# Kernel tuning notes

Hardware: AMD Instinct MI355X
Metric: run time of the kernel (lower is better)

Reference implementation:

```python
import jax, jax.numpy as jnp
import numpy as np

N = 100000      # nodes
E = 1600000     # edges
F_IN = 128      # feature_dim
H = 128         # hidden_dim
OUT = 40        # out_dim


def setup_inputs() -> dict:
    key = jax.random.key(0)
    ks = jax.random.split(key, 8)
    x = jax.random.normal(ks[0], (N, F_IN), dtype=jnp.float32)
    edge_index = jax.random.randint(ks[1], (2, E), 0, N)
    def lin(k, fan_in, fan_out):
        kw, kb = jax.random.split(k)
        s = 1.0 / np.sqrt(fan_in)
        W = jax.random.uniform(kw, (fan_in, fan_out), jnp.float32, -s, s)
        b = jax.random.uniform(kb, (fan_out,), jnp.float32, -s, s)
        return W, b
    W1, b1 = lin(ks[2], F_IN, H)
    W2, b2 = lin(ks[3], H, H)
    Wc, bc = lin(ks[4], H, OUT)
    return {"x": x, "W1": W1, "b1": b1, "W2": W2, "b2": b2,
            "Wc": Wc, "bc": bc, "edge_index": edge_index}


def gcn_conv(x, W, b, src, dst, n):
    # GCNConv: D^{-1/2} (A + I) D^{-1/2} X W + b  (self loops already in src/dst)
    h = x @ W                                            # [n, out]
    deg = jax.ops.segment_sum(jnp.ones(src.shape[0], h.dtype), dst,
                              num_segments=n)            # [n]
    dinv = jnp.where(deg > 0, jax.lax.rsqrt(deg), 0.0)
    norm = dinv[src] * dinv[dst]                         # [E+n]
    msg = h[src] * norm[:, None]                         # gather + scale
    out = jax.ops.segment_sum(msg, dst, num_segments=n)  # scatter-add
    return out + b


def reference(x, W1, b1, W2, b2, Wc, bc, edge_index):
    loops = jnp.arange(N, dtype=edge_index.dtype)
    src = jnp.concatenate([edge_index[0], loops])
    dst = jnp.concatenate([edge_index[1], loops])
    # mode=0, eval mode: dropout is identity
    out1 = jax.nn.relu(gcn_conv(x, W1, b1, src, dst, N))
    out2 = jax.nn.relu(gcn_conv(out1, W2, b2, src, dst, N))
    return (out2 + out1) @ Wc + bc
```

## Files before the change

### kernel.cpp

```cpp
#include <hip/hip_runtime.h>
#include <stdint.h>


#define HID 128
#define OUTD 40
#define BSH 8
#define BCAP 6144
#define CAPSH 13
#define EPB 8192
#define NBMAX 512

typedef __attribute__((ext_vector_type(8))) short short8;
typedef __attribute__((ext_vector_type(4))) float f32x4;
typedef __attribute__((ext_vector_type(2))) float f32x2;

__device__ inline uint16_t f32_to_bf16(float f) {
    uint32_t u = __float_as_uint(f);
    uint32_t r = u + 0x7FFFu + ((u >> 16) & 1u);
    return (uint16_t)(r >> 16);
}
__device__ inline uint32_t pack_bf16x2(float lo, float hi) {
    return (uint32_t)f32_to_bf16(lo) | ((uint32_t)f32_to_bf16(hi) << 16);
}
__device__ inline float bf_lo(uint32_t u) { return __uint_as_float(u << 16); }
__device__ inline float bf_hi(uint32_t u) { return __uint_as_float(u & 0xFFFF0000u); }
__device__ inline f32x2 up2(uint32_t u) {
    f32x2 r;
    r.x = __uint_as_float(u << 16);
    r.y = __uint_as_float(u & 0xFFFF0000u);
    return r;
}


__global__ __launch_bounds__(256) void gnn_bucket_scatter_k(const int* __restrict__ edges,
                                                            int* __restrict__ pcur,
                                                            uint32_t* __restrict__ pairbuf,
                                                            int E, int NB) {
    __shared__ int hist[NBMAX];
    int e0 = blockIdx.x * EPB;
    int e1 = min(E, e0 + EPB);
    for (int b = threadIdx.x; b < NB; b += 256) hist[b] = 0;
    __syncthreads();
    for (int e = e0 + threadIdx.x; e < e1; e += 256)
        atomicAdd(&hist[edges[E + e] >> BSH], 1);
    __syncthreads();
    for (int b = threadIdx.x; b < NB; b += 256) {
        int c = hist[b];
        hist[b] = (c > 0) ? (atomicAdd(&pcur[b], c) + (b << CAPSH)) : 0;
    }
    __syncthreads();
    for (int e = e0 + threadIdx.x; e < e1; e += 256) {
        int src = edges[e];
        int dst = edges[E + e];
        int pos = atomicAdd(&hist[dst >> BSH], 1);
        pairbuf[pos] = ((uint32_t)(dst & 255) << 24) | (uint32_t)src;
    }
}

__global__ __launch_bounds__(512) void gnn_scan_wsw_k(const int* __restrict__ pcur,
                                                      int* __restrict__ bucketoff,
                                                      const float* __restrict__ W1,
                                                      const float* __restrict__ W2,
                                                      uint16_t* __restrict__ w1s,
                                                      uint16_t* __restrict__ w2s,
                                                      int n, int NB) {
    if (blockIdx.x == 0) {
        __shared__ int s[512];
        int t = threadIdx.x;
        int v = 0;
        if (t < NB) v = pcur[t] + min(256, n - (t << BSH));
        s[t] = v;
        __syncthreads();
        for (int off = 1; off < 512; off <<= 1) {
            int x = 0;
            if (t >= off) x = s[t - off];
            __syncthreads();
            if (t >= off) s[t] += x;
            __syncthreads();
        }
        if (t <= NB) bucketoff[t] = s[t] - v;
    } else if (threadIdx.x < 256) {
        int wb = blockIdx.x - 1;
        const float* W = (wb < 8) ? W1 : W2;
        uint16_t* O = (wb < 8) ? w1s : w2s;
        int t = (wb & 7) * 256 + threadIdx.x;
        int lane = t & 63;
        int ksct = t >> 6;
        int nn = (ksct >> 2) * 16 + (lane & 15);
        int k0 = (ksct & 3) * 32 + (lane >> 4) * 8;
        uint32_t d[4];
#pragma unroll
        for (int j = 0; j < 4; ++j)
            d[j] = pack_bf16x2(W[(size_t)(k0 + 2 * j) * HID + nn],
                               W[(size_t)(k0 + 2 * j + 1) * HID + nn]);
        *(uint4*)(O + (size_t)t * 8) = make_uint4(d[0], d[1], d[2], d[3]);
    }
}

__global__ __launch_bounds__(256) void gnn_build_csr_k(const uint32_t* __restrict__ pairbuf,
                                                       const int* __restrict__ bucketoff,
                                                       int* __restrict__ rowptr,
                                                       float* __restrict__ dinv,
                                                       int* __restrict__ colidx, int n) {
    __shared__ int deg[256];
    __shared__ int scn[256];
    __shared__ int colbuf[BCAP];
    int b = blockIdx.x;
    int nb0 = b << BSH;
    int nb1 = min(n, nb0 + 256);
    int nn = nb1 - nb0;
    int segbeg = bucketoff[b];
    int segend = bucketoff[b + 1];
    int seglen = segend - segbeg;
    int pairbeg = b << CAPSH;
    int npairs = seglen - nn;
    int t = threadIdx.x;

    deg[t] = 0;
    __syncthreads();
    for (int p = t; p < npairs; p += 256)
        atomicAdd(&deg[pairbuf[pairbeg + p] >> 24], 1);
    __syncthreads();

    int d = (t < nn) ? deg[t] : 0;
    int v = (t < nn) ? d + 1 : 0;
    scn[t] = v;
    __syncthreads();
    for (int off = 1; off < 256; off <<= 1) {
        int x = 0;
        if (t >= off) x = scn[t - off];
        __syncthreads();
        if (t >= off) scn[t] += x;
        __syncthreads();
    }
    int rel = scn[t] - v;
    if (t < nn) {
        rowptr[nb0 + t + 1] = segbeg + scn[t];
        dinv[nb0 + t] = rsqrtf((float)(d + 1));
    }
    if (t == 0) rowptr[nb0] = segbeg;
    __syncthreads();

    if (seglen <= BCAP) {
        if (t < nn) {
            colbuf[rel] = nb0 + t;
            deg[t] = rel + 1;
        }
        __syncthreads();
        for (int p = t; p < npairs; p += 256) {
            uint32_t pr = pairbuf[pairbeg + p];
            int pos = atomicAdd(&deg[pr >> 24], 1);
            colbuf[pos] = (int)(pr & 0xFFFFFFu);
        }
        __syncthreads();
        for (int i = t; i < seglen; i += 256)
            colidx[segbeg + i] = colbuf[i];
    } else {
        if (t < nn) {
            colidx[segbeg + rel] = nb0 + t;
            deg[t] = rel + 1;
        }
        __syncthreads();
        for (int p = t; p < npairs; p += 256) {
            uint32_t pr = pairbuf[pairbeg + p];
            int pos = atomicAdd(&deg[pr >> 24], 1);
            colidx[segbeg + pos] = (int)(pr & 0xFFFFFFu);
        }
    }
}


template <bool ABF16>
__global__ __launch_bounds__(256) void gnn_gemm_mfma_k(const void* __restrict__ Aptr,
                                                       const uint32_t* __restrict__ Wsw,
                                                       const float* __restrict__ dinv,
                                                       uint16_t* __restrict__ outh, int n) {
    int wave = threadIdx.x >> 6;
    int lane = threadIdx.x & 63;
    int m = lane & 15;
    int q = lane >> 4;
    int row0 = blockIdx.x * 64 + wave * 16;
    int arow = min(row0 + m, n - 1);

    f32x4 acc[8];
#pragma unroll
    for (int i = 0; i < 8; ++i) acc[i] = (f32x4){0.f, 0.f, 0.f, 0.f};

#pragma unroll
    for (int ks = 0; ks < 4; ++ks) {
        short8 a;
        if (ABF16) {
            const uint16_t* Ab = (const uint16_t*)Aptr;
            uint4 u = *(const uint4*)(Ab + (size_t)arow * HID + ks * 32 + q * 8);
            a = __builtin_bit_cast(short8, u);
        } else {
            const float* Af = (const float*)Aptr + (size_t)arow * HID + ks * 32 + q * 8;
            uint4 u0 = *(const uint4*)(Af);
            uint4 u1 = *(const uint4*)(Af + 4);
            uint4 p;
            p.x = pack_bf16x2(__uint_as_float(u0.x), __uint_as_float(u0.y));
            p.y = pack_bf16x2(__uint_as_float(u0.z), __uint_as_float(u0.w));
            p.z = pack_bf16x2(__uint_as_float(u1.x), __uint_as_float(u1.y));
            p.w = pack_bf16x2(__uint_as_float(u1.z), __uint_as_float(u1.w));
            a = __builtin_bit_cast(short8, p);
        }
#pragma unroll
        for (int ct = 0; ct < 8; ++ct) {
            uint4 bu = *(const uint4*)(Wsw + ((size_t)(ct * 4 + ks) * 64 + lane) * 4);
            short8 bfr = __builtin_bit_cast(short8, bu);
            acc[ct] = __builtin_amdgcn_mfma_f32_16x16x32_bf16(a, bfr, acc[ct], 0, 0, 0);
        }
    }

    float dv[4];
#pragma unroll
    for (int r = 0; r < 4; ++r) dv[r] = dinv[min(row0 + q * 4 + r, n - 1)];

#pragma unroll
    for (int ct = 0; ct < 8; ++ct) {
#pragma unroll
        for (int r = 0; r < 4; ++r) {
            int rr = row0 + q * 4 + r;
            if (rr < n)
                outh[(size_t)rr * HID + ct * 16 + m] = f32_to_bf16(acc[ct][r] * dv[r]);
        }
    }
}


__global__ __launch_bounds__(256) void gnn_aggregate_k(const uint4* __restrict__ h4,
                                const int* __restrict__ rowptr,
                                const int* __restrict__ colidx, const float* __restrict__ dinv,
                                const float* __restrict__ bias,
                                const uint16_t* __restrict__ skipb,
                                uint16_t* __restrict__ outsh, int n) {
    int node = blockIdx.x * 4 + (threadIdx.x >> 6);
    if (node >= n) return;
    int lane = threadIdx.x & 63;
    int g = lane >> 4;
    int sub = lane & 15;
    int beg = rowptr[node];
    int end = rowptr[node + 1];
    f32x2 acc2[4];
#pragma unroll
    for (int i = 0; i < 4; ++i) acc2[i] = (f32x2){0.f, 0.f};
    int e = beg;
    for (; e + 15 < end; e += 16) {
        int j0 = colidx[e + g];
        int j1 = colidx[e + 4 + g];
        int j2 = colidx[e + 8 + g];
        int j3 = colidx[e + 12 + g];
        uint4 u0 = h4[(size_t)j0 * 16 + sub];
        uint4 u1 = h4[(size_t)j1 * 16 + sub];
        uint4 u2 = h4[(size_t)j2 * 16 + sub];
        uint4 u3 = h4[(size_t)j3 * 16 + sub];
        acc2[0] += up2(u0.x); acc2[1] += up2(u0.y); acc2[2] += up2(u0.z); acc2[3] += up2(u0.w);
        acc2[0] += up2(u1.x); acc2[1] += up2(u1.y); acc2[2] += up2(u1.z); acc2[3] += up2(u1.w);
        acc2[0] += up2(u2.x); acc2[1] += up2(u2.y); acc2[2] += up2(u2.z); acc2[3] += up2(u2.w);
        acc2[0] += up2(u3.x); acc2[1] += up2(u3.y); acc2[2] += up2(u3.z); acc2[3] += up2(u3.w);
    }
    for (; e + 3 < end; e += 4) {
        int j = colidx[e + g];
        uint4 u = h4[(size_t)j * 16 + sub];
        acc2[0] += up2(u.x); acc2[1] += up2(u.y); acc2[2] += up2(u.z); acc2[3] += up2(u.w);
    }
    if (g < end - e) {
        int j = colidx[e + g];
        uint4 u = h4[(size_t)j * 16 + sub];
        acc2[0] += up2(u.x); acc2[1] += up2(u.y); acc2[2] += up2(u.z); acc2[3] += up2(u.w);
    }
    float a8[8];
#pragma unroll
    for (int i = 0; i < 4; ++i) { a8[2 * i] = acc2[i].x; a8[2 * i + 1] = acc2[i].y; }
#pragma unroll
    for (int k = 0; k < 8; ++k) {
        a8[k] += __shfl_xor(a8[k], 16, 64);
        a8[k] += __shfl_xor(a8[k], 32, 64);
    }
    if (lane < 32) {
        int half = lane >> 4;
        int col = sub * 8 + half * 4;
        float di = dinv[node];
        float4 bv = *(const float4*)(bias + col);
        float o0 = fmaxf(di * a8[half * 4 + 0] + bv.x, 0.0f);
        float o1 = fmaxf(di * a8[half * 4 + 1] + bv.y, 0.0f);
        float o2 = fmaxf(di * a8[half * 4 + 2] + bv.z, 0.0f);
        float o3 = fmaxf(di * a8[half * 4 + 3] + bv.w, 0.0f);
        if (skipb) {
            uint2 sv = *(const uint2*)(skipb + (size_t)node * HID + col);
            o0 += bf_lo(sv.x); o1 += bf_hi(sv.x);
            o2 += bf_lo(sv.y); o3 += bf_hi(sv.y);
        }
        uint2 sh;
        sh.x = pack_bf16x2(o0, o1);
        sh.y = pack_bf16x2(o2, o3);
        *(uint2*)(outsh + (size_t)node * HID + col) = sh;
    }
}


__global__ __launch_bounds__(320) void gnn_final_k(const uint16_t* __restrict__ sumh,
                                                   const float* __restrict__ wc,
                                                   const float* __restrict__ bc,
                                                   float* __restrict__ out, int n) {
    __shared__ float a[64 * HID];
    const int tx = threadIdx.x % 10;
    const int ty = threadIdx.x / 10;
    const int row0 = blockIdx.x * 64;

    {
        const uint4* S8 = (const uint4*)sumh;
        float4* s4 = (float4*)a;
        for (int idx = threadIdx.x; idx < 64 * 16; idx += 320) {
            int r = idx >> 4, c8 = idx & 15;
            uint4 v = make_uint4(0u, 0u, 0u, 0u);
            if (row0 + r < n) v = S8[(size_t)(row0 + r) * 16 + c8];
            float4 f0 = make_float4(bf_lo(v.x), bf_hi(v.x), bf_lo(v.y), bf_hi(v.y));
            float4 f1 = make_float4(bf_lo(v.z), bf_hi(v.z), bf_lo(v.w), bf_hi(v.w));
            s4[r * 32 + ((2 * c8) ^ (r & 7))] = f0;
            s4[r * 32 + ((2 * c8 + 1) ^ (r & 7))] = f1;
        }
    }
    __syncthreads();

    float acc[2][4];
    {
        float b0 = bc[tx * 4], b1 = bc[tx * 4 + 1], b2 = bc[tx * 4 + 2], b3 = bc[tx * 4 + 3];
        acc[0][0] = b0; acc[0][1] = b1; acc[0][2] = b2; acc[0][3] = b3;
        acc[1][0] = b0; acc[1][1] = b1; acc[1][2] = b2; acc[1][3] = b3;
    }
    const float* wp = wc + tx * 4;
    const float4* s4 = (const float4*)a;

#pragma unroll 2
    for (int k = 0; k < HID; k += 4) {
        int c4 = k >> 2;
        float ar[2][4];
#pragma unroll
        for (int r = 0; r < 2; ++r) {
            int row = ty * 2 + r;
            *(float4*)&ar[r][0] = s4[row * 32 + (c4 ^ (row & 7))];
        }
#pragma unroll
        for (int kk = 0; kk < 4; ++kk) {
            float4 w = *(const float4*)(wp + (size_t)(k + kk) * OUTD);
#pragma unroll
            for (int r = 0; r < 2; ++r) {
                acc[r][0] += ar[r][kk] * w.x;
                acc[r][1] += ar[r][kk] * w.y;
                acc[r][2] += ar[r][kk] * w.z;
                acc[r][3] += ar[r][kk] * w.w;
            }
        }
    }

#pragma unroll
    for (int r = 0; r < 2; ++r) {
        int row = row0 + ty * 2 + r;
        if (row < n) {
            float4 v = make_float4(acc[r][0], acc[r][1], acc[r][2], acc[r][3]);
            *(float4*)(out + (size_t)row * OUTD + tx * 4) = v;
        }
    }
}


extern "C" void kernel_launch(void* const* d_in, const int* in_sizes, int n_in,
                              void* d_out, int out_size, void* d_ws, size_t ws_size,
                              hipStream_t stream) {
    const int N = in_sizes[0] / HID;
    const int E = in_sizes[7] / 2;

    const float* x  = (const float*)d_in[0];
    const float* W1 = (const float*)d_in[1];
    const float* b1 = (const float*)d_in[2];
    const float* W2 = (const float*)d_in[3];
    const float* b2 = (const float*)d_in[4];
    const float* Wc = (const float*)d_in[5];
    const float* bc = (const float*)d_in[6];
    const int* edges = (const int*)d_in[7];
    float* out = (float*)d_out;

    char* w = (char*)d_ws;
    auto alloc = [&](size_t bytes) -> char* {
        char* p = w;
        w += (bytes + 255) & ~(size_t)255;
        return p;
    };
    uint16_t* hbuf  = (uint16_t*)alloc((size_t)N * HID * 2);
    uint16_t* bufBh = (uint16_t*)alloc((size_t)N * HID * 2);
    int*   rowptr  = (int*)alloc((size_t)(N + 1) * 4);
    int*   colidx  = (int*)alloc((size_t)(E + N) * 4);
    float* dinv    = (float*)alloc((size_t)N * 4);
    int*   pcur      = (int*)alloc(512 * 4);
    int*   bucketoff = (int*)alloc(513 * 4);
    uint16_t* w1s  = (uint16_t*)alloc(HID * HID * 2);
    uint16_t* w2s  = (uint16_t*)alloc(HID * HID * 2);

    uint32_t* pairbuf = (uint32_t*)hbuf;

    const int NB = (N + 255) >> BSH;
    const int nEB = (E + EPB - 1) / EPB;

    hipMemsetAsync(pcur, 0, 512 * 4, stream);

    gnn_bucket_scatter_k<<<nEB, 256, 0, stream>>>(edges, pcur, pairbuf, E, NB);
    gnn_scan_wsw_k<<<17, 512, 0, stream>>>(pcur, bucketoff, W1, W2, w1s, w2s, N, NB);
    gnn_build_csr_k<<<NB, 256, 0, stream>>>(pairbuf, bucketoff, rowptr, dinv, colidx, N);

    gnn_gemm_mfma_k<false><<<(N + 63) / 64, 256, 0, stream>>>(x, (const uint32_t*)w1s, dinv, hbuf, N);
    gnn_aggregate_k<<<(N + 3) / 4, 256, 0, stream>>>((const uint4*)hbuf, rowptr, colidx,
                                                     dinv, b1, nullptr, bufBh, N);
    gnn_gemm_mfma_k<true><<<(N + 63) / 64, 256, 0, stream>>>(bufBh, (const uint32_t*)w2s, dinv, hbuf, N);
    gnn_aggregate_k<<<(N + 3) / 4, 256, 0, stream>>>((const uint4*)hbuf, rowptr, colidx,
                                                     dinv, b2, bufBh, bufBh, N);
    gnn_final_k<<<(N + 63) / 64, 320, 0, stream>>>(bufBh, Wc, bc, out, N);
}
```

Measured before the change: 357.9 us.

## Fuse scan into CSR build, weight swizzle into scatter, head into aggregate

Merges the edge bucket scatter and the bf16 weight swizzle into one launch. Drops the separate scan kernel by having each CSR-build block reduce the preceding bucket counts itself. Fuses the final 128x40 classifier into the second aggregation: per-node outputs are staged in shared memory and 40 lanes compute the dot products, so the bf16 skip-sum buffer is never written or re-read. This removes two launches and one full-tensor round trip, at the cost of redundant prefix reductions per block and a less efficient per-wave head matmul reading Wc from global memory.

Result: slower. 366.6 us (+2.4%).

```diff
diff --git a/kernel.cpp b/kernel.cpp
--- a/kernel.cpp
+++ b/kernel.cpp
@@ -31,56 +31,16 @@
     return r;
 }
 
-
-__global__ __launch_bounds__(256) void gnn_bucket_scatter_k(const int* __restrict__ edges,
-                                                            int* __restrict__ pcur,
-                                                            uint32_t* __restrict__ pairbuf,
-                                                            int E, int NB) {
-    __shared__ int hist[NBMAX];
-    int e0 = blockIdx.x * EPB;
-    int e1 = min(E, e0 + EPB);
-    for (int b = threadIdx.x; b < NB; b += 256) hist[b] = 0;
-    __syncthreads();
-    for (int e = e0 + threadIdx.x; e < e1; e += 256)
-        atomicAdd(&hist[edges[E + e] >> BSH], 1);
-    __syncthreads();
-    for (int b = threadIdx.x; b < NB; b += 256) {
-        int c = hist[b];
-        hist[b] = (c > 0) ? (atomicAdd(&pcur[b], c) + (b << CAPSH)) : 0;
-    }
-    __syncthreads();
-    for (int e = e0 + threadIdx.x; e < e1; e += 256) {
-        int src = edges[e];
-        int dst = edges[E + e];
-        int pos = atomicAdd(&hist[dst >> BSH], 1);
-        pairbuf[pos] = ((uint32_t)(dst & 255) << 24) | (uint32_t)src;
-    }
-}
-
-__global__ __launch_bounds__(512) void gnn_scan_wsw_k(const int* __restrict__ pcur,
-                                                      int* __restrict__ bucketoff,
-                                                      const float* __restrict__ W1,
-                                                      const float* __restrict__ W2,
-                                                      uint16_t* __restrict__ w1s,
-                                                      uint16_t* __restrict__ w2s,
-                                                      int n, int NB) {
-    if (blockIdx.x == 0) {
-        __shared__ int s[512];
-        int t = threadIdx.x;
-        int v = 0;
-        if (t < NB) v = pcur[t] + min(256, n - (t << BSH));
-        s[t] = v;
-        __syncthreads();
-        for (int off = 1; off < 512; off <<= 1) {
-            int x = 0;
-            if (t >= off) x = s[t - off];
-            __syncthreads();
-            if (t >= off) s[t] += x;
-            __syncthreads();
-        }
-        if (t <= NB) bucketoff[t] = s[t] - v;
-    } else if (threadIdx.x < 256) {
-        int wb = blockIdx.x - 1;
+__global__ __launch_bounds__(256) void gnn_scatter_wsw_k(const int* __restrict__ edges,
+                                                         int* __restrict__ pcur,
+                                                         uint32_t* __restrict__ pairbuf,
+                                                         const float* __restrict__ W1,
+                                                         const float* __restrict__ W2,
+                                                         uint16_t* __restrict__ w1s,
+                                                         uint16_t* __restrict__ w2s,
+                                                         int E, int NB, int nEB) {
+    if ((int)blockIdx.x >= nEB) {
+        int wb = blockIdx.x - nEB;
         const float* W = (wb < 8) ? W1 : W2;
         uint16_t* O = (wb < 8) ? w1s : w2s;
         int t = (wb & 7) * 256 + threadIdx.x;
@@ -94,27 +54,57 @@
             d[j] = pack_bf16x2(W[(size_t)(k0 + 2 * j) * HID + nn],
                                W[(size_t)(k0 + 2 * j + 1) * HID + nn]);
         *(uint4*)(O + (size_t)t * 8) = make_uint4(d[0], d[1], d[2], d[3]);
+        return;
+    }
+    __shared__ int hist[NBMAX];
+    int e0 = blockIdx.x * EPB;
+    int e1 = min(E, e0 + EPB);
+    for (int b = threadIdx.x; b < NB; b += 256) hist[b] = 0;
+    __syncthreads();
+    for (int e = e0 + threadIdx.x; e < e1; e += 256)
+        atomicAdd(&hist[edges[E + e] >> BSH], 1);
+    __syncthreads();
+    for (int b = threadIdx.x; b < NB; b += 256) {
+        int c = hist[b];
+        hist[b] = (c > 0) ? (atomicAdd(&pcur[b], c) + (b << CAPSH)) : 0;
+    }
+    __syncthreads();
+    for (int e = e0 + threadIdx.x; e < e1; e += 256) {
+        int src = edges[e];
+        int dst = edges[E + e];
+        int pos = atomicAdd(&hist[dst >> BSH], 1);
+        pairbuf[pos] = ((uint32_t)(dst & 255) << 24) | (uint32_t)src;
     }
 }
 
 __global__ __launch_bounds__(256) void gnn_build_csr_k(const uint32_t* __restrict__ pairbuf,
-                                                       const int* __restrict__ bucketoff,
+                                                       const int* __restrict__ pcur,
                                                        int* __restrict__ rowptr,
                                                        float* __restrict__ dinv,
                                                        int* __restrict__ colidx, int n) {
+    __shared__ int red[256];
     __shared__ int deg[256];
     __shared__ int scn[256];
     __shared__ int colbuf[BCAP];
     int b = blockIdx.x;
+    int t = threadIdx.x;
+
+    int part = 0;
+    for (int i = t; i < b; i += 256) part += pcur[i];
+    red[t] = part;
+    __syncthreads();
+    for (int off = 128; off > 0; off >>= 1) {
+        if (t < off) red[t] += red[t + off];
+        __syncthreads();
+    }
+    const int segbeg = red[0] + (b << BSH);
+
     int nb0 = b << BSH;
     int nb1 = min(n, nb0 + 256);
     int nn = nb1 - nb0;
-    int segbeg = bucketoff[b];
-    int segend = bucketoff[b + 1];
-    int seglen = segend - segbeg;
+    int npairs = pcur[b];
+    int seglen = npairs + nn;
     int pairbeg = b << CAPSH;
-    int npairs = seglen - nn;
-    int t = threadIdx.x;
 
     deg[t] = 0;
     __syncthreads();
@@ -228,13 +218,19 @@
 }
 
 
+template <bool FUSE_HEAD>
 __global__ __launch_bounds__(256) void gnn_aggregate_k(const uint4* __restrict__ h4,
                                 const int* __restrict__ rowptr,
                                 const int* __restrict__ colidx, const float* __restrict__ dinv,
                                 const float* __restrict__ bias,
                                 const uint16_t* __restrict__ skipb,
-                                uint16_t* __restrict__ outsh, int n) {
-    int node = blockIdx.x * 4 + (threadIdx.x >> 6);
+                                uint16_t* __restrict__ outsh,
+                                const float* __restrict__ wc,
+                                const float* __restrict__ bc,
+                                float* __restrict__ outf, int n) {
+    __shared__ float srow[4][HID];
+    int wv = threadIdx.x >> 6;
+    int node = blockIdx.x * 4 + wv;
     if (node >= n) return;
     int lane = threadIdx.x & 63;
     int g = lane >> 4;
@@ -291,75 +287,28 @@
             o0 += bf_lo(sv.x); o1 += bf_hi(sv.x);
             o2 += bf_lo(sv.y); o3 += bf_hi(sv.y);
         }
-        uint2 sh;
-        sh.x = pack_bf16x2(o0, o1);
-        sh.y = pack_bf16x2(o2, o3);
-        *(uint2*)(outsh + (size_t)node * HID + col) = sh;
-    }
-}
-
-
-__global__ __launch_bounds__(320) void gnn_final_k(const uint16_t* __restrict__ sumh,
-                                                   const float* __restrict__ wc,
-                                                   const float* __restrict__ bc,
-                                                   float* __restrict__ out, int n) {
-    __shared__ float a[64 * HID];
-    const int tx = threadIdx.x % 10;
-    const int ty = threadIdx.x / 10;
-    const int row0 = blockIdx.x * 64;
-
-    {
-        const uint4* S8 = (const uint4*)sumh;
-        float4* s4 = (float4*)a;
-        for (int idx = threadIdx.x; idx < 64 * 16; idx += 320) {
-            int r = idx >> 4, c8 = idx & 15;
-            uint4 v = make_uint4(0u, 0u, 0u, 0u);
-            if (row0 + r < n) v = S8[(size_t)(row0 + r) * 16 + c8];
-            float4 f0 = make_float4(bf_lo(v.x), bf_hi(v.x), bf_lo(v.y), bf_hi(v.y));
-            float4 f1 = make_float4(bf_lo(v.z), bf_hi(v.z), bf_lo(v.w), bf_hi(v.w));
-            s4[r * 32 + ((2 * c8) ^ (r & 7))] = f0;
-            s4[r * 32 + ((2 * c8 + 1) ^ (r & 7))] = f1;
-        }
-    }
-    __syncthreads();
-
-    float acc[2][4];
-    {
-        float b0 = bc[tx * 4], b1 = bc[tx * 4 + 1], b2 = bc[tx * 4 + 2], b3 = bc[tx * 4 + 3];
-        acc[0][0] = b0; acc[0][1] = b1; acc[0][2] = b2; acc[0][3] = b3;
-        acc[1][0] = b0; acc[1][1] = b1; acc[1][2] = b2; acc[1][3] = b3;
-    }
-    const float* wp = wc + tx * 4;
-    const float4* s4 = (const float4*)a;
-
-#pragma unroll 2
-    for (int k = 0; k < HID; k += 4) {
-        int c4 = k >> 2;
-        float ar[2][4];
-#pragma unroll
-        for (int r = 0; r < 2; ++r) {
-            int row = ty * 2 + r;
-            *(float4*)&ar[r][0] = s4[row * 32 + (c4 ^ (row & 7))];
-        }
-#pragma unroll
-        for (int kk = 0; kk < 4; ++kk) {
-            float4 w = *(const float4*)(wp + (size_t)(k + kk) * OUTD);
-#pragma unroll
-            for (int r = 0; r < 2; ++r) {
-                acc[r][0] += ar[r][kk] * w.x;
-                acc[r][1] += ar[r][kk] * w.y;
-                acc[r][2] += ar[r][kk] * w.z;
-                acc[r][3] += ar[r][kk] * w.w;
+        if (!FUSE_HEAD) {
+            uint2 sh;
+            sh.x = pack_bf16x2(o0, o1);
+            sh.y = pack_bf16x2(o2, o3);
+            *(uint2*)(outsh + (size_t)node * HID + col) = sh;
+        } else {
+            *(float4*)&srow[wv][col] = make_float4(o0, o1, o2, o3);
+        }
+    }
+    if (FUSE_HEAD) {
+        if (lane < OUTD) {
+            float acc = bc[lane];
+            const float4* s4 = (const float4*)srow[wv];
+#pragma unroll 4
+            for (int k4 = 0; k4 < HID / 4; ++k4) {
+                float4 sv = s4[k4];
+                acc += sv.x * wc[(size_t)(k4 * 4 + 0) * OUTD + lane];
+                acc += sv.y * wc[(size_t)(k4 * 4 + 1) * OUTD + lane];
+                acc += sv.z * wc[(size_t)(k4 * 4 + 2) * OUTD + lane];
+                acc += sv.w * wc[(size_t)(k4 * 4 + 3) * OUTD + lane];
             }
-        }
-    }
-
-#pragma unroll
-    for (int r = 0; r < 2; ++r) {
-        int row = row0 + ty * 2 + r;
-        if (row < n) {
-            float4 v = make_float4(acc[r][0], acc[r][1], acc[r][2], acc[r][3]);
-            *(float4*)(out + (size_t)row * OUTD + tx * 4) = v;
+            outf[(size_t)node * OUTD + lane] = acc;
         }
     }
 }
@@ -392,8 +341,7 @@
     int*   rowptr  = (int*)alloc((size_t)(N + 1) * 4);
     int*   colidx  = (int*)alloc((size_t)(E + N) * 4);
     float* dinv    = (float*)alloc((size_t)N * 4);
-    int*   pcur      = (int*)alloc(512 * 4);
-    int*   bucketoff = (int*)alloc(513 * 4);
+    int*   pcur    = (int*)alloc(512 * 4);
     uint16_t* w1s  = (uint16_t*)alloc(HID * HID * 2);
     uint16_t* w2s  = (uint16_t*)alloc(HID * HID * 2);
 
@@ -404,15 +352,16 @@
 
     hipMemsetAsync(pcur, 0, 512 * 4, stream);
 
-    gnn_bucket_scatter_k<<<nEB, 256, 0, stream>>>(edges, pcur, pairbuf, E, NB);
-    gnn_scan_wsw_k<<<17, 512, 0, stream>>>(pcur, bucketoff, W1, W2, w1s, w2s, N, NB);
-    gnn_build_csr_k<<<NB, 256, 0, stream>>>(pairbuf, bucketoff, rowptr, dinv, colidx, N);
+    gnn_scatter_wsw_k<<<nEB + 16, 256, 0, stream>>>(edges, pcur, pairbuf,
+                                                    W1, W2, w1s, w2s, E, NB, nEB);
+    gnn_build_csr_k<<<NB, 256, 0, stream>>>(pairbuf, pcur, rowptr, dinv, colidx, N);
 
     gnn_gemm_mfma_k<false><<<(N + 63) / 64, 256, 0, stream>>>(x, (const uint32_t*)w1s, dinv, hbuf, N);
-    gnn_aggregate_k<<<(N + 3) / 4, 256, 0, stream>>>((const uint4*)hbuf, rowptr, colidx,
-                                                     dinv, b1, nullptr, bufBh, N);
+    gnn_aggregate_k<false><<<(N + 3) / 4, 256, 0, stream>>>((const uint4*)hbuf, rowptr, colidx,
+                                                            dinv, b1, nullptr, bufBh,
+                                                            nullptr, nullptr, nullptr, N);
     gnn_gemm_mfma_k<true><<<(N + 63) / 64, 256, 0, stream>>>(bufBh, (const uint32_t*)w2s, dinv, hbuf, N);
-    gnn_aggregate_k<<<(N + 3) / 4, 256, 0, stream>>>((const uint4*)hbuf, rowptr, colidx,
-                                                     dinv, b2, bufBh, bufBh, N);
-    gnn_final_k<<<(N + 63) / 64, 320, 0, stream>>>(bufBh, Wc, bc, out, N);
-}
+    gnn_aggregate_k<true><<<(N + 3) / 4, 256, 0, stream>>>((const uint4*)hbuf, rowptr, colidx,
+                                                           dinv, b2, bufBh, nullptr,
+                                                           Wc, bc, out, N);
+}
```
